# Optimization experiments

Hardware: AMD Instinct MI355X
Metric: run time of the kernel (lower is better)

Reference implementation:

```python
import jax, jax.numpy as jnp
import numpy as np

N = 1_000_000          # number of RoIs
C = 4                  # num_class (foreground classes)
IMG_H, IMG_W = 1080.0, 1920.0
BBOX_MEAN = jnp.array([0.0, 0.0, 0.0, 0.0], jnp.float32)
BBOX_STD = jnp.array([0.1, 0.1, 0.2, 0.2], jnp.float32)
THR_OBJ = 0.2          # threshold_objectness
THR_CLS = 0.1          # thresholds[0]
MIN_W, MIN_H = 6.0, 6.0
MAX_CAND = 300         # nms max_candidate_n
OVERLAP = 0.5          # nms overlap_ratio
TOP_N = 100            # nms top_n


def setup_inputs() -> dict:
    key = jax.random.key(0)
    k1, k2, k3, k4, k5 = jax.random.split(key, 5)
    logits = jax.random.normal(k1, (N, C + 1), jnp.float32) * 2.0
    cls_score_softmax = jax.nn.softmax(logits, axis=-1)          # rows sum to 1, like softmax output
    bbox_pred = jax.random.normal(k2, (N, 4 * (C + 1)), jnp.float32) * 0.5
    x1 = jax.random.uniform(k3, (N,), jnp.float32, 0.0, IMG_W * 0.8)
    y1 = jax.random.uniform(k4, (N,), jnp.float32, 0.0, IMG_H * 0.8)
    wh = jax.random.uniform(k5, (N, 2), jnp.float32, 8.0, 200.0)
    rois = jnp.stack([jnp.zeros((N,), jnp.float32), x1, y1, x1 + wh[:, 0], y1 + wh[:, 1]], axis=1)
    im_info = jnp.array([IMG_H, IMG_W], jnp.float32)
    return {"cls_score_softmax": cls_score_softmax, "bbox_pred": bbox_pred, "rois": rois, "im_info": im_info}


def _pairwise_iou(b):
    # torchvision box_iou convention: area = (x2-x1)*(y2-y1), no +1
    lt = jnp.maximum(b[:, None, :2], b[None, :, :2])
    rb = jnp.minimum(b[:, None, 2:], b[None, :, 2:])
    wh = jnp.clip(rb - lt, 0.0)
    inter = wh[..., 0] * wh[..., 1]
    area = (b[:, 2] - b[:, 0]) * (b[:, 3] - b[:, 1])
    return inter / (area[:, None] + area[None, :] - inter)


def _forward(cls_score_softmax, bbox_pred, rois, im_info):
    h_img, w_img = im_info[0], im_info[1]
    # denormalize deltas and decode against rois (bbox_transform_inv_rcnn)
    deltas = (bbox_pred.reshape(-1, 4) * BBOX_STD + BBOX_MEAN).reshape(-1, C + 1, 4)
    bx = rois[:, 1:]
    w = bx[:, 2] - bx[:, 0] + 1.0
    h = bx[:, 3] - bx[:, 1] + 1.0
    cx = bx[:, 0] + 0.5 * (w - 1.0)
    cy = bx[:, 1] + 0.5 * (h - 1.0)
    pcx = deltas[:, :, 0] * w[:, None] + cx[:, None]
    pcy = deltas[:, :, 1] * h[:, None] + cy[:, None]
    pw = jnp.exp(deltas[:, :, 2]) * w[:, None]
    ph = jnp.exp(deltas[:, :, 3]) * h[:, None]
    pred = jnp.stack([pcx - 0.5 * (pw - 1.0), pcy - 0.5 * (ph - 1.0),
                      pcx + 0.5 * (pw - 1.0), pcy + 0.5 * (ph - 1.0)], axis=-1)  # [N, C+1, 4]
    # refine_out_of_map_bbox: clip to image
    pred = jnp.stack([jnp.clip(pred[..., 0], 0.0, w_img - 1.0),
                      jnp.clip(pred[..., 1], 0.0, h_img - 1.0),
                      jnp.clip(pred[..., 2], 0.0, w_img - 1.0),
                      jnp.clip(pred[..., 3], 0.0, h_img - 1.0)], axis=-1)
    # objectness + class-score filters (masked instead of compacted: jit-friendly)
    mask_obj = (1.0 - cls_score_softmax[:, 0]) >= THR_OBJ
    maxes = jnp.max(cls_score_softmax[:, 1:], axis=1)
    argmaxes = jnp.argmax(cls_score_softmax[:, 1:], axis=1) + 1
    mask_cls = maxes > THR_CLS
    # select the box of the argmax class per row
    box = jnp.take_along_axis(pred, argmaxes[:, None, None], axis=1)[:, 0, :]  # [N, 4]
    bw = box[:, 2] - box[:, 0] + 1.0
    bh = box[:, 3] - box[:, 1] + 1.0
    mask_size = (bw >= MIN_W) | (bh >= MIN_H)  # HEIGHT_OR_WIDTH
    valid = mask_obj & mask_cls & mask_size
    # top-k candidates by max class prob (invalid rows pushed below any real score)
    cand_scores = jnp.where(valid, maxes, -1.0)
    top_vals, top_idx = jax.lax.top_k(cand_scores, MAX_CAND)   # sorted descending
    cand_boxes = box[top_idx]                                   # [M, 4]
    cand_probs = cls_score_softmax[top_idx]                     # [M, C+1]
    cand_valid = top_vals > -0.5
    # greedy NMS over the (score-sorted) candidates
    iou = _pairwise_iou(cand_boxes)
    idx = jnp.arange(MAX_CAND)

    def body(i, keep):
        sup = keep[i] & (iou[i] > OVERLAP) & (idx > i)
        return keep & ~sup

    keep = jax.lax.fori_loop(0, MAX_CAND, body, cand_valid)
    # compact kept rows into the first TOP_N slots (drop-row scatter trick)
    order = jnp.cumsum(keep.astype(jnp.int32)) - 1
    slot = jnp.where(keep & (order < TOP_N), order, TOP_N)
    rows = jnp.concatenate([jnp.zeros((MAX_CAND, 1), cand_boxes.dtype), cand_boxes, cand_probs], axis=1)
    out = jnp.zeros((TOP_N + 1, rows.shape[1]), rows.dtype).at[slot].set(rows)[:TOP_N]
    return out  # [TOP_N, 1 + 4 + (C+1)] = [100, 10], zero-padded past the kept count


def reference(cls_score_softmax, bbox_pred, rois, im_info):
    return _forward(cls_score_softmax, bbox_pred, rois, im_info)
```

## Files before the change

kernel.cpp:

```cpp
#include <hip/hip_runtime.h>
#include <math.h>

#define NBINS 4096
#define CAP   4096
#define MAXC  300
#define MAXCP 320
#define TOPN  100

__device__ __forceinline__ int bin_of(float s) {
    int b = (int)(s * (float)NBINS);
    return b > NBINS-1 ? NBINS-1 : b;
}
__device__ __forceinline__ int subbin_of(float s, int tau) {
    float f = s * (float)NBINS - (float)tau;
    int sb = (int)(f * (float)NBINS);
    sb = sb < 0 ? 0 : (sb > NBINS-1 ? NBINS-1 : sb);
    return sb;
}

__device__ __forceinline__ unsigned long long rdlane64(unsigned long long v, int lane) {
    unsigned int lo = (unsigned int)__builtin_amdgcn_readlane((int)(unsigned int)(v & 0xFFFFFFFFull), lane);
    unsigned int hi = (unsigned int)__builtin_amdgcn_readlane((int)(unsigned int)(v >> 32), lane);
    return ((unsigned long long)hi << 32) | (unsigned long long)lo;
}

__device__ __forceinline__ void decode4(float x1, float y1, float x2, float y2,
                                        float4 d4, float Wimg, float Himg,
                                        float& bx1, float& by1, float& bx2, float& by2)
{
    float w  = x2 - x1 + 1.0f;
    float h  = y2 - y1 + 1.0f;
    float cx = x1 + 0.5f*(w - 1.0f);
    float cy = y1 + 0.5f*(h - 1.0f);
    float d0 = d4.x*0.1f, d1 = d4.y*0.1f, d2 = d4.z*0.2f, d3 = d4.w*0.2f;
    float pcx = d0*w + cx;
    float pcy = d1*h + cy;
    float pw  = expf(d2)*w;
    float ph  = expf(d3)*h;
    bx1 = fminf(fmaxf(pcx - 0.5f*(pw-1.0f), 0.0f), Wimg-1.0f);
    by1 = fminf(fmaxf(pcy - 0.5f*(ph-1.0f), 0.0f), Himg-1.0f);
    bx2 = fminf(fmaxf(pcx + 0.5f*(pw-1.0f), 0.0f), Wimg-1.0f);
    by2 = fminf(fmaxf(pcy + 0.5f*(ph-1.0f), 0.0f), Himg-1.0f);
}

__global__ __launch_bounds__(256)
void rcnn_pass1(const float4* __restrict__ cls4, const float4* __restrict__ bbox4,
                const float4* __restrict__ rois4, const float* __restrict__ iminfo,
                float4* __restrict__ scores4,
                unsigned int* __restrict__ hist, unsigned int* __restrict__ hist2,
                unsigned int* __restrict__ counter, int Ng)
{
    if (blockIdx.x == 0) {
        for (int k = threadIdx.x; k < NBINS; k += 256) { hist[k] = 0u; hist2[k] = 0u; }
        if (threadIdx.x == 0) *counter = 0u;
    }

    int g = blockIdx.x * blockDim.x + threadIdx.x;
    if (g >= Ng) return;

    float c[20], q[20];
    #pragma unroll
    for (int v = 0; v < 5; v++) {
        float4 cv = cls4[5*g + v];
        c[4*v] = cv.x; c[4*v+1] = cv.y; c[4*v+2] = cv.z; c[4*v+3] = cv.w;
        float4 rv = rois4[5*g + v];
        q[4*v] = rv.x; q[4*v+1] = rv.y; q[4*v+2] = rv.z; q[4*v+3] = rv.w;
    }
    float Himg = iminfo[0], Wimg = iminfo[1];

    float s[4];
    #pragma unroll
    for (int j = 0; j < 4; j++) {
        float p0 = c[5*j], p1 = c[5*j+1], p2 = c[5*j+2], p3 = c[5*j+3], p4 = c[5*j+4];
        float m = p1; int a = 1;
        if (p2 > m) { m = p2; a = 2; }
        if (p3 > m) { m = p3; a = 3; }
        if (p4 > m) { m = p4; a = 4; }
        float sc = -1.0f;
        if (((1.0f - p0) >= 0.2f) && (m > 0.1f)) {
            float4 d4 = bbox4[20*g + 5*j + a];
            float bx1, by1, bx2, by2;
            decode4(q[5*j+1], q[5*j+2], q[5*j+3], q[5*j+4], d4, Wimg, Himg, bx1, by1, bx2, by2);
            float bw = bx2 - bx1 + 1.0f;
            float bh = by2 - by1 + 1.0f;
            if ((bw >= 6.0f) || (bh >= 6.0f)) sc = m;
        }
        s[j] = sc;
    }
    scores4[g] = make_float4(s[0], s[1], s[2], s[3]);
}

__global__ __launch_bounds__(1024)
void rcnn_hist(const float4* __restrict__ scores4, unsigned int* __restrict__ hist, int Ng)
{
    __shared__ unsigned int lh[NBINS];
    const int t = threadIdx.x;
    for (int k = t; k < NBINS; k += 1024) lh[k] = 0u;
    __syncthreads();
    int stride = gridDim.x * 1024;
    for (int g = blockIdx.x * 1024 + t; g < Ng; g += stride) {
        float4 s4 = scores4[g];
        float ss[4] = { s4.x, s4.y, s4.z, s4.w };
        #pragma unroll
        for (int j = 0; j < 4; j++)
            if (ss[j] > -0.5f) atomicAdd(&lh[bin_of(ss[j])], 1u);
    }
    __syncthreads();
    for (int k = t; k < NBINS; k += 1024) {
        unsigned int v = lh[k];
        if (v) atomicAdd(&hist[k], v);
    }
}

__global__ __launch_bounds__(1024)
void rcnn_pass2(const unsigned int* __restrict__ hist, int* __restrict__ taubin)
{
    __shared__ unsigned int suf[1024];
    __shared__ int g_sh;
    int t = threadIdx.x;
    suf[t] = hist[4*t] + hist[4*t+1] + hist[4*t+2] + hist[4*t+3];
    __syncthreads();
    for (int d = 1; d < 1024; d <<= 1) {
        unsigned int add = (t + d < 1024) ? suf[t + d] : 0u;
        __syncthreads();
        suf[t] += add;
        __syncthreads();
    }
    if (t == 0) g_sh = -1;
    __syncthreads();
    if (suf[t] >= MAXC && (t == 1023 || suf[t+1] < MAXC)) g_sh = t;
    __syncthreads();
    if (t == 0) {
        int g = g_sh;
        int tau = 0;
        if (g >= 0) {
            unsigned int cum = (g == 1023) ? 0u : suf[g+1];
            tau = 4*g;
            for (int k = 3; k >= 0; k--) {
                cum += hist[4*g + k];
                if (cum >= MAXC) { tau = 4*g + k; break; }
            }
        }
        *taubin = tau;
    }
}

__global__ __launch_bounds__(1024)
void rcnn_hist2(const float4* __restrict__ scores4, const int* __restrict__ taubin,
                unsigned int* __restrict__ hist2, int Ng)
{
    __shared__ unsigned int lh[NBINS];
    const int t = threadIdx.x;
    const int tau = *taubin;
    for (int k = t; k < NBINS; k += 1024) lh[k] = 0u;
    __syncthreads();
    int stride = gridDim.x * 1024;
    for (int g = blockIdx.x * 1024 + t; g < Ng; g += stride) {
        float4 s4 = scores4[g];
        float ss[4] = { s4.x, s4.y, s4.z, s4.w };
        #pragma unroll
        for (int j = 0; j < 4; j++)
            if (ss[j] > -0.5f && bin_of(ss[j]) == tau)
                atomicAdd(&lh[subbin_of(ss[j], tau)], 1u);
    }
    __syncthreads();
    for (int k = t; k < NBINS; k += 1024) {
        unsigned int v = lh[k];
        if (v) atomicAdd(&hist2[k], v);
    }
}

__global__ __launch_bounds__(1024)
void rcnn_pass2b(const unsigned int* __restrict__ hist, const unsigned int* __restrict__ hist2,
                 const int* __restrict__ taubin, int* __restrict__ tau2out)
{
    __shared__ unsigned int red[1024];
    __shared__ unsigned int suf[1024];
    __shared__ int g_sh;
    __shared__ unsigned int need_sh;
    int t = threadIdx.x;
    int tau = *taubin;
    unsigned int acc = 0;
    for (int k = tau + 1 + t; k < NBINS; k += 1024) acc += hist[k];
    red[t] = acc;
    __syncthreads();
    for (int d = 512; d > 0; d >>= 1) { if (t < d) red[t] += red[t + d]; __syncthreads(); }
    if (t == 0) {
        unsigned int C1 = red[0];
        need_sh = (C1 >= MAXC) ? 1u : (unsigned int)(MAXC - C1);
    }
    __syncthreads();
    unsigned int need = need_sh;
    suf[t] = hist2[4*t] + hist2[4*t+1] + hist2[4*t+2] + hist2[4*t+3];
    __syncthreads();
    for (int d = 1; d < 1024; d <<= 1) {
        unsigned int add = (t + d < 1024) ? suf[t + d] : 0u;
        __syncthreads();
        suf[t] += add;
        __syncthreads();
    }
    if (t == 0) g_sh = -1;
    __syncthreads();
    if (suf[t] >= need && (t == 1023 || suf[t+1] < need)) g_sh = t;
    __syncthreads();
    if (t == 0) {
        int g = g_sh;
        int tau2 = 0;
        if (g >= 0) {
            unsigned int cum = (g == 1023) ? 0u : suf[g+1];
            tau2 = 4*g;
            for (int k = 3; k >= 0; k--) {
                cum += hist2[4*g + k];
                if (cum >= need) { tau2 = 4*g + k; break; }
            }
        }
        *tau2out = tau2;
    }
}

__global__ __launch_bounds__(256)
void rcnn_pass3(const float4* __restrict__ scores4, const int* __restrict__ taubin,
                const int* __restrict__ tau2bin,
                unsigned long long* __restrict__ ckey,
                unsigned int* __restrict__ counter, int Ng)
{
    int g = blockIdx.x * blockDim.x + threadIdx.x;
    if (g >= Ng) return;
    float4 s4 = scores4[g];
    int tau = *taubin, tau2 = *tau2bin;
    float ss[4] = { s4.x, s4.y, s4.z, s4.w };
    #pragma unroll
    for (int j = 0; j < 4; j++) {
        float s = ss[j];
        if (s > -0.5f) {
            int bin = bin_of(s);
            bool sel = (bin > tau) || (bin == tau && subbin_of(s, tau) >= tau2);
            if (sel) {
                unsigned int pos = atomicAdd(counter, 1u);
                if (pos < CAP) {
                    unsigned int idx = (unsigned int)(4*g + j);
                    ckey[pos] = ((unsigned long long)__float_as_uint(s) << 32)
                              | (unsigned long long)(~idx);
                }
            }
        }
    }
}

__global__ __launch_bounds__(1024)
void rcnn_final(const float* __restrict__ cls, const float* __restrict__ bbox,
                const float* __restrict__ rois, const float* __restrict__ iminfo,
                const unsigned long long* __restrict__ ckey,
                const unsigned int* __restrict__ counter, float* __restrict__ out)
{
    __shared__ unsigned long long skey[CAP];
    __shared__ int    tid_[MAXC];
    __shared__ float4 bx4[MAXCP];
    __shared__ float  pr_[MAXC][5];
    __shared__ unsigned long long sup[MAXC][5];
    __shared__ unsigned long long maskw[5];
    __shared__ float orows[TOPN*10];
    const int t  = threadIdx.x;
    const int NT = 1024;
    int M = (int)*counter; if (M > CAP) M = CAP;

    for (int i = t; i < M; i += NT)  skey[i] = ckey[i];
    for (int r = t; r < MAXC; r += NT) tid_[r] = -1;
    for (int r = t; r < MAXCP; r += NT) bx4[r] = make_float4(0.f, 0.f, 0.f, 0.f);
    if (t < 5) maskw[t] = 0ull;
    for (int k = t; k < TOPN*10; k += NT) orows[k] = 0.0f;
    __syncthreads();

    for (int i = t; i < M; i += NT) {
        unsigned long long ki = skey[i];
        int r = 0;
        for (int j = 0; j < M; j++) r += (skey[j] > ki);
        if (r < MAXC) tid_[r] = (int)(~(unsigned int)ki);
    }
    __syncthreads();

    float Himg = iminfo[0], Wimg = iminfo[1];
    for (int r = t; r < MAXC; r += NT) {
        int i = tid_[r];
        if (i >= 0) {
            float p0 = cls[5*i], p1 = cls[5*i+1], p2 = cls[5*i+2], p3 = cls[5*i+3], p4 = cls[5*i+4];
            pr_[r][0]=p0; pr_[r][1]=p1; pr_[r][2]=p2; pr_[r][3]=p3; pr_[r][4]=p4;
            float m = p1; int a = 1;
            if (p2 > m) { m = p2; a = 2; }
            if (p3 > m) { m = p3; a = 3; }
            if (p4 > m) { m = p4; a = 4; }
            float4 d4 = ((const float4*)bbox)[5*i + a];
            float bx1, by1, bx2, by2;
            decode4(rois[5*i+1], rois[5*i+2], rois[5*i+3], rois[5*i+4], d4, Wimg, Himg, bx1, by1, bx2, by2);
            bx4[r] = make_float4(bx1, by1, bx2, by2);
            atomicOr(&maskw[r>>6], 1ull << (r & 63));
        }
    }
    __syncthreads();

    for (int task = t; task < MAXC*5; task += NT) {
        int w = task / MAXC;
        int i = task - w*MAXC;
        unsigned long long bits = 0ull;
        int j0 = w << 6;
        if (j0 + 63 > i) {
            float4 A = bx4[i];
            float areaA = (A.z - A.x)*(A.w - A.y);
            for (int b = 0; b < 64; b++) {
                float4 B = bx4[j0 + b];
                float lx = fmaxf(A.x, B.x), ly = fmaxf(A.y, B.y);
                float rx = fminf(A.z, B.z), ry = fminf(A.w, B.w);
                float iw = fmaxf(rx - lx, 0.0f), ih = fmaxf(ry - ly, 0.0f);
                float inter = iw * ih;
                float areaB = (B.z - B.x)*(B.w - B.y);
                float iou = inter / (areaA + areaB - inter);
                bits |= (iou > 0.5f) ? (1ull << b) : 0ull;
            }
            unsigned long long jgt = (i < j0) ? ~0ull
                                  : ((i - j0) >= 63 ? 0ull : ~((1ull << (i - j0 + 1)) - 1ull));
            bits &= jgt & maskw[w];
        }
        sup[i][w] = bits;
    }
    __syncthreads();

    if (t < 64) {
        unsigned long long S0[5], S1[5], S2[5], S3[5], S4[5];
        #pragma unroll
        for (int w = 0; w < 5; w++) {
            S0[w] = sup[t][w];
            S1[w] = sup[64 + t][w];
            S2[w] = sup[128 + t][w];
            S3[w] = sup[192 + t][w];
            S4[w] = (t < MAXC - 256) ? sup[256 + t][w] : 0ull;
        }
        unsigned long long kw0 = maskw[0], kw1 = maskw[1], kw2 = maskw[2],
                           kw3 = maskw[3], kw4 = maskw[4];
#define SCAN_SET(S, kwr, COUNT)                                             \
        for (int s2 = 0; s2 < (COUNT); s2++) {                              \
            unsigned long long m = ((kwr >> s2) & 1ull) ? ~0ull : 0ull;     \
            kw0 &= ~(rdlane64(S[0], s2) & m);                               \
            kw1 &= ~(rdlane64(S[1], s2) & m);                               \
            kw2 &= ~(rdlane64(S[2], s2) & m);                               \
            kw3 &= ~(rdlane64(S[3], s2) & m);                               \
            kw4 &= ~(rdlane64(S[4], s2) & m);                               \
        }
        SCAN_SET(S0, kw0, 64)
        SCAN_SET(S1, kw1, 64)
        SCAN_SET(S2, kw2, 64)
        SCAN_SET(S3, kw3, 64)
        SCAN_SET(S4, kw4, MAXC - 256)
#undef SCAN_SET
        if (t == 0) {
            maskw[0] = kw0; maskw[1] = kw1; maskw[2] = kw2;
            maskw[3] = kw3; maskw[4] = kw4;
        }
    }
    __syncthreads();

    for (int r = t; r < MAXC; r += NT) {
        if ((maskw[r>>6] >> (r & 63)) & 1ull) {
            int ord = 0;
            for (int w2 = 0; w2 < (r >> 6); w2++) ord += __popcll(maskw[w2]);
            ord += __popcll(maskw[r>>6] & ((1ull << (r & 63)) - 1ull));
            if (ord < TOPN) {
                float* row = &orows[ord*10];
                float4 B = bx4[r];
                row[0] = 0.0f;
                row[1] = B.x; row[2] = B.y; row[3] = B.z; row[4] = B.w;
                row[5] = pr_[r][0]; row[6] = pr_[r][1]; row[7] = pr_[r][2];
                row[8] = pr_[r][3]; row[9] = pr_[r][4];
            }
        }
    }
    __syncthreads();
    for (int k = t; k < TOPN*10; k += NT) out[k] = orows[k];
}

extern "C" void kernel_launch(void* const* d_in, const int* in_sizes, int n_in,
                              void* d_out, int out_size, void* d_ws, size_t ws_size,
                              hipStream_t stream)
{
    const float* cls    = (const float*)d_in[0];
    const float* bbox   = (const float*)d_in[1];
    const float* rois   = (const float*)d_in[2];
    const float* iminfo = (const float*)d_in[3];
    int N  = in_sizes[0] / 5;
    int Ng = N / 4;

    char* ws = (char*)d_ws;
    float* scores = (float*)ws;
    size_t off = ((size_t)N * 4 + 255) & ~(size_t)255;
    unsigned int* hist    = (unsigned int*)(ws + off); off += NBINS * 4;
    unsigned int* hist2   = (unsigned int*)(ws + off); off += NBINS * 4;
    int*          taubin  = (int*)(ws + off);          off += 256;
    int*          tau2bin = (int*)(ws + off);          off += 256;
    unsigned int* counter = (unsigned int*)(ws + off); off += 256;
    unsigned long long* ckey = (unsigned long long*)(ws + off); off += CAP * 8;

    int blocksG = (Ng + 255) / 256;
    rcnn_pass1<<<blocksG, 256, 0, stream>>>((const float4*)cls, (const float4*)bbox,
                                            (const float4*)rois, iminfo,
                                            (float4*)scores, hist, hist2, counter, Ng);
    rcnn_hist<<<64, 1024, 0, stream>>>((const float4*)scores, hist, Ng);
    rcnn_pass2<<<1, 1024, 0, stream>>>(hist, taubin);
    rcnn_hist2<<<64, 1024, 0, stream>>>((const float4*)scores, taubin, hist2, Ng);
    rcnn_pass2b<<<1, 1024, 0, stream>>>(hist, hist2, taubin, tau2bin);
    rcnn_pass3<<<blocksG, 256, 0, stream>>>((const float4*)scores, taubin, tau2bin,
                                            ckey, counter, Ng);
    rcnn_final<<<1, 1024, 0, stream>>>(cls, bbox, rois, iminfo,
                                       ckey, counter, (float*)d_out);
}
```

Before: 225.1 us.

## Split final stage into prep kernel and single-wave NMS scan kernel

Splits the single-block final kernel into a 1024-thread prep kernel, which ranks candidates, decodes boxes and builds suppression bitmasks into global workspace, and a 64-thread single-wave kernel, which runs the serial readlane NMS scan and compacts the output rows. In the old kernel the serial scan ran inside a 1024-thread block with heavy LDS use, and the intent is to give it a lean launch that may get better register allocation and less wasted occupancy. The emit step now uses per-lane popcount prefixes across five blocks instead of per-thread loops. In exchange it adds one extra kernel launch and a round trip of the intermediate data through global memory.

New measurement: 229.2 us. No clear change (+1.9%).

```diff
diff --git a/kernel.cpp b/kernel.cpp
--- a/kernel.cpp
+++ b/kernel.cpp
@@ -248,18 +248,19 @@
 }
 
 __global__ __launch_bounds__(1024)
-void rcnn_final(const float* __restrict__ cls, const float* __restrict__ bbox,
-                const float* __restrict__ rois, const float* __restrict__ iminfo,
-                const unsigned long long* __restrict__ ckey,
-                const unsigned int* __restrict__ counter, float* __restrict__ out)
+void rcnn_prep(const float* __restrict__ cls, const float* __restrict__ bbox,
+               const float* __restrict__ rois, const float* __restrict__ iminfo,
+               const unsigned long long* __restrict__ ckey,
+               const unsigned int* __restrict__ counter,
+               unsigned long long* __restrict__ sup_g,
+               float4* __restrict__ bx4_g,
+               float* __restrict__ pr_g,
+               unsigned long long* __restrict__ maskw_g)
 {
     __shared__ unsigned long long skey[CAP];
     __shared__ int    tid_[MAXC];
     __shared__ float4 bx4[MAXCP];
-    __shared__ float  pr_[MAXC][5];
-    __shared__ unsigned long long sup[MAXC][5];
     __shared__ unsigned long long maskw[5];
-    __shared__ float orows[TOPN*10];
     const int t  = threadIdx.x;
     const int NT = 1024;
     int M = (int)*counter; if (M > CAP) M = CAP;
@@ -268,7 +269,6 @@
     for (int r = t; r < MAXC; r += NT) tid_[r] = -1;
     for (int r = t; r < MAXCP; r += NT) bx4[r] = make_float4(0.f, 0.f, 0.f, 0.f);
     if (t < 5) maskw[t] = 0ull;
-    for (int k = t; k < TOPN*10; k += NT) orows[k] = 0.0f;
     __syncthreads();
 
     for (int i = t; i < M; i += NT) {
@@ -283,8 +283,10 @@
     for (int r = t; r < MAXC; r += NT) {
         int i = tid_[r];
         if (i >= 0) {
-            float p0 = cls[5*i], p1 = cls[5*i+1], p2 = cls[5*i+2], p3 = cls[5*i+3], p4 = cls[5*i+4];
-            pr_[r][0]=p0; pr_[r][1]=p1; pr_[r][2]=p2; pr_[r][3]=p3; pr_[r][4]=p4;
+            pr_g[5*r+0] = cls[5*i];   pr_g[5*r+1] = cls[5*i+1];
+            pr_g[5*r+2] = cls[5*i+2]; pr_g[5*r+3] = cls[5*i+3];
+            pr_g[5*r+4] = cls[5*i+4];
+            float p1 = cls[5*i+1], p2 = cls[5*i+2], p3 = cls[5*i+3], p4 = cls[5*i+4];
             float m = p1; int a = 1;
             if (p2 > m) { m = p2; a = 2; }
             if (p3 > m) { m = p3; a = 3; }
@@ -292,11 +294,15 @@
             float4 d4 = ((const float4*)bbox)[5*i + a];
             float bx1, by1, bx2, by2;
             decode4(rois[5*i+1], rois[5*i+2], rois[5*i+3], rois[5*i+4], d4, Wimg, Himg, bx1, by1, bx2, by2);
-            bx4[r] = make_float4(bx1, by1, bx2, by2);
+            float4 B = make_float4(bx1, by1, bx2, by2);
+            bx4[r] = B;
+            bx4_g[r] = B;
             atomicOr(&maskw[r>>6], 1ull << (r & 63));
         }
     }
     __syncthreads();
+
+    if (t < 5) maskw_g[t] = maskw[t];
 
     for (int task = t; task < MAXC*5; task += NT) {
         int w = task / MAXC;
@@ -320,61 +326,82 @@
                                   : ((i - j0) >= 63 ? 0ull : ~((1ull << (i - j0 + 1)) - 1ull));
             bits &= jgt & maskw[w];
         }
-        sup[i][w] = bits;
-    }
-    __syncthreads();
-
-    if (t < 64) {
-        unsigned long long S0[5], S1[5], S2[5], S3[5], S4[5];
-        #pragma unroll
-        for (int w = 0; w < 5; w++) {
-            S0[w] = sup[t][w];
-            S1[w] = sup[64 + t][w];
-            S2[w] = sup[128 + t][w];
-            S3[w] = sup[192 + t][w];
-            S4[w] = (t < MAXC - 256) ? sup[256 + t][w] : 0ull;
-        }
-        unsigned long long kw0 = maskw[0], kw1 = maskw[1], kw2 = maskw[2],
-                           kw3 = maskw[3], kw4 = maskw[4];
-#define SCAN_SET(S, kwr, COUNT)                                             \
-        for (int s2 = 0; s2 < (COUNT); s2++) {                              \
-            unsigned long long m = ((kwr >> s2) & 1ull) ? ~0ull : 0ull;     \
-            kw0 &= ~(rdlane64(S[0], s2) & m);                               \
-            kw1 &= ~(rdlane64(S[1], s2) & m);                               \
-            kw2 &= ~(rdlane64(S[2], s2) & m);                               \
-            kw3 &= ~(rdlane64(S[3], s2) & m);                               \
-            kw4 &= ~(rdlane64(S[4], s2) & m);                               \
-        }
-        SCAN_SET(S0, kw0, 64)
-        SCAN_SET(S1, kw1, 64)
-        SCAN_SET(S2, kw2, 64)
-        SCAN_SET(S3, kw3, 64)
-        SCAN_SET(S4, kw4, MAXC - 256)
-#undef SCAN_SET
-        if (t == 0) {
-            maskw[0] = kw0; maskw[1] = kw1; maskw[2] = kw2;
-            maskw[3] = kw3; maskw[4] = kw4;
-        }
-    }
-    __syncthreads();
-
-    for (int r = t; r < MAXC; r += NT) {
-        if ((maskw[r>>6] >> (r & 63)) & 1ull) {
-            int ord = 0;
-            for (int w2 = 0; w2 < (r >> 6); w2++) ord += __popcll(maskw[w2]);
-            ord += __popcll(maskw[r>>6] & ((1ull << (r & 63)) - 1ull));
-            if (ord < TOPN) {
-                float* row = &orows[ord*10];
-                float4 B = bx4[r];
-                row[0] = 0.0f;
-                row[1] = B.x; row[2] = B.y; row[3] = B.z; row[4] = B.w;
-                row[5] = pr_[r][0]; row[6] = pr_[r][1]; row[7] = pr_[r][2];
-                row[8] = pr_[r][3]; row[9] = pr_[r][4];
-            }
-        }
-    }
-    __syncthreads();
-    for (int k = t; k < TOPN*10; k += NT) out[k] = orows[k];
+        sup_g[i*5 + w] = bits;
+    }
+}
+
+__global__ __launch_bounds__(64, 1)
+void rcnn_nms(const unsigned long long* __restrict__ sup_g,
+              const float4* __restrict__ bx4_g,
+              const float* __restrict__ pr_g,
+              const unsigned long long* __restrict__ maskw_g,
+              float* __restrict__ out)
+{
+    __shared__ float orows[TOPN*10];
+    const int l = threadIdx.x;
+
+    unsigned long long A0 = sup_g[l*5+0], A1 = sup_g[l*5+1], A2 = sup_g[l*5+2],
+                       A3 = sup_g[l*5+3], A4 = sup_g[l*5+4];
+    unsigned long long B0 = sup_g[(64+l)*5+0], B1 = sup_g[(64+l)*5+1], B2 = sup_g[(64+l)*5+2],
+                       B3 = sup_g[(64+l)*5+3], B4 = sup_g[(64+l)*5+4];
+    unsigned long long C0 = sup_g[(128+l)*5+0], C1 = sup_g[(128+l)*5+1], C2 = sup_g[(128+l)*5+2],
+                       C3 = sup_g[(128+l)*5+3], C4 = sup_g[(128+l)*5+4];
+    unsigned long long D0 = sup_g[(192+l)*5+0], D1 = sup_g[(192+l)*5+1], D2 = sup_g[(192+l)*5+2],
+                       D3 = sup_g[(192+l)*5+3], D4 = sup_g[(192+l)*5+4];
+    bool e = (l < MAXC - 256);
+    unsigned long long E0 = e ? sup_g[(256+l)*5+0] : 0ull,
+                       E1 = e ? sup_g[(256+l)*5+1] : 0ull,
+                       E2 = e ? sup_g[(256+l)*5+2] : 0ull,
+                       E3 = e ? sup_g[(256+l)*5+3] : 0ull,
+                       E4 = e ? sup_g[(256+l)*5+4] : 0ull;
+
+    unsigned long long kw0 = maskw_g[0], kw1 = maskw_g[1], kw2 = maskw_g[2],
+                       kw3 = maskw_g[3], kw4 = maskw_g[4];
+
+#define SCAN_BLK(W0, W1, W2, W3, W4, KWREF, COUNT)                          \
+    for (int s2 = 0; s2 < (COUNT); s2++) {                                  \
+        unsigned long long m = ((KWREF >> s2) & 1ull) ? ~0ull : 0ull;       \
+        kw0 &= ~(rdlane64(W0, s2) & m);                                     \
+        kw1 &= ~(rdlane64(W1, s2) & m);                                     \
+        kw2 &= ~(rdlane64(W2, s2) & m);                                     \
+        kw3 &= ~(rdlane64(W3, s2) & m);                                     \
+        kw4 &= ~(rdlane64(W4, s2) & m);                                     \
+    }
+    SCAN_BLK(A0, A1, A2, A3, A4, kw0, 64)
+    SCAN_BLK(B0, B1, B2, B3, B4, kw1, 64)
+    SCAN_BLK(C0, C1, C2, C3, C4, kw2, 64)
+    SCAN_BLK(D0, D1, D2, D3, D4, kw3, 64)
+    SCAN_BLK(E0, E1, E2, E3, E4, kw4, MAXC - 256)
+#undef SCAN_BLK
+
+    for (int k = l; k < TOPN*10; k += 64) orows[k] = 0.0f;
+    __syncthreads();
+
+    int p0 = __popcll(kw0), p1 = __popcll(kw1), p2 = __popcll(kw2), p3 = __popcll(kw3);
+    unsigned long long lmask = (l == 0) ? 0ull : ((~0ull) >> (64 - l));
+
+#define EMIT_BLK(KW, BASE, PRE)                                             \
+    if ((KW >> l) & 1ull) {                                                 \
+        int r   = (BASE) + l;                                               \
+        int ord = (PRE) + __popcll(KW & lmask);                             \
+        if (ord < TOPN) {                                                   \
+            float4 B = bx4_g[r];                                            \
+            float* row = &orows[ord*10];                                    \
+            row[0] = 0.0f;                                                  \
+            row[1] = B.x; row[2] = B.y; row[3] = B.z; row[4] = B.w;         \
+            row[5] = pr_g[5*r+0]; row[6] = pr_g[5*r+1];                     \
+            row[7] = pr_g[5*r+2]; row[8] = pr_g[5*r+3];                     \
+            row[9] = pr_g[5*r+4];                                           \
+        }                                                                   \
+    }
+    EMIT_BLK(kw0,   0, 0)
+    EMIT_BLK(kw1,  64, p0)
+    EMIT_BLK(kw2, 128, p0 + p1)
+    EMIT_BLK(kw3, 192, p0 + p1 + p2)
+    if (l < MAXC - 256) { EMIT_BLK(kw4, 256, p0 + p1 + p2 + p3) }
+#undef EMIT_BLK
+    __syncthreads();
+    for (int k = l; k < TOPN*10; k += 64) out[k] = orows[k];
 }
 
 extern "C" void kernel_launch(void* const* d_in, const int* in_sizes, int n_in,
@@ -396,7 +423,11 @@
     int*          taubin  = (int*)(ws + off);          off += 256;
     int*          tau2bin = (int*)(ws + off);          off += 256;
     unsigned int* counter = (unsigned int*)(ws + off); off += 256;
-    unsigned long long* ckey = (unsigned long long*)(ws + off); off += CAP * 8;
+    unsigned long long* ckey   = (unsigned long long*)(ws + off); off += CAP * 8;
+    unsigned long long* sup_g  = (unsigned long long*)(ws + off); off += MAXC * 5 * 8 + 64;
+    float4*             bx4_g  = (float4*)(ws + off);             off += MAXC * 16 + 64;
+    float*              pr_g   = (float*)(ws + off);              off += MAXC * 5 * 4 + 64;
+    unsigned long long* maskw_g= (unsigned long long*)(ws + off); off += 64;
 
     int blocksG = (Ng + 255) / 256;
     rcnn_pass1<<<blocksG, 256, 0, stream>>>((const float4*)cls, (const float4*)bbox,
@@ -408,6 +439,7 @@
     rcnn_pass2b<<<1, 1024, 0, stream>>>(hist, hist2, taubin, tau2bin);
     rcnn_pass3<<<blocksG, 256, 0, stream>>>((const float4*)scores, taubin, tau2bin,
                                             ckey, counter, Ng);
-    rcnn_final<<<1, 1024, 0, stream>>>(cls, bbox, rois, iminfo,
-                                       ckey, counter, (float*)d_out);
-}
+    rcnn_prep<<<1, 1024, 0, stream>>>(cls, bbox, rois, iminfo, ckey, counter,
+                                      sup_g, bx4_g, pr_g, maskw_g);
+    rcnn_nms<<<1, 64, 0, stream>>>(sup_g, bx4_g, pr_g, maskw_g, (float*)d_out);
+}
```
